# Kernel tuning notes

Measured on AMD Instinct MI355X. Metric: run time of the kernel, lower is better.

## Reference

```python
import jax, jax.numpy as jnp
import numpy as np

B, S, D, H, L = 32, 64, 8, 256, 2


def _lstm_layer(x, Wih, Whh, b):
    # x: (B, S, Hin) -> outputs (B, S, H), final h, c (B, H). PyTorch gate order i,f,g,o.
    Bsz = x.shape[0]
    Hd = Whh.shape[1]
    h0 = jnp.zeros((Bsz, Hd), x.dtype)
    c0 = jnp.zeros((Bsz, Hd), x.dtype)

    def step(carry, xt):
        h, c = carry
        g = xt @ Wih.T + h @ Whh.T + b
        i, f, gg, o = jnp.split(g, 4, axis=-1)
        c = jax.nn.sigmoid(f) * c + jax.nn.sigmoid(i) * jnp.tanh(gg)
        h = jax.nn.sigmoid(o) * jnp.tanh(c)
        return (h, c), h

    (hT, cT), ys = jax.lax.scan(step, (h0, c0), jnp.swapaxes(x, 0, 1))
    return jnp.swapaxes(ys, 0, 1), hT, cT


def _encode(x, layers):
    hs, cs = [], []
    out = x
    for (Wih, Whh, b) in layers:
        out, hT, cT = _lstm_layer(out, Wih, Whh, b)
        hs.append(hT)
        cs.append(cT)
    return out, jnp.stack(hs), jnp.stack(cs)  # out (B,S,H), h/c (L,B,H)


def _cell_step(x, h, c, layers):
    # single time-step through stacked LSTM. x (B,H); h,c (L,B,H)
    hs, cs = [], []
    inp = x
    for l, (Wih, Whh, b) in enumerate(layers):
        g = inp @ Wih.T + h[l] @ Whh.T + b
        i, f, gg, o = jnp.split(g, 4, axis=-1)
        cn = jax.nn.sigmoid(f) * c[l] + jax.nn.sigmoid(i) * jnp.tanh(gg)
        hn = jax.nn.sigmoid(o) * jnp.tanh(cn)
        hs.append(hn)
        cs.append(cn)
        inp = hn
    return inp, jnp.stack(hs), jnp.stack(cs)


def setup_inputs() -> dict:
    key = jax.random.key(0)
    ks = jax.random.split(key, 24)
    s = 0.05
    inputs = jax.random.uniform(ks[0], (B, S, D), dtype=jnp.float32)
    inputs = inputs.at[..., -1].set(0.0)  # is_visited flag starts at 0
    p = {}
    p['inputs'] = inputs
    p['W_emb'] = jax.random.normal(ks[1], (H, D), jnp.float32) * s
    p['b_emb'] = jax.random.normal(ks[2], (H,), jnp.float32) * s
    i = 3
    for pref, in0 in (('enc', H), ('dec', H)):
        for l in range(L):
            p[f'{pref}_Wih{l}'] = jax.random.normal(ks[i], (4 * H, in0 if l == 0 else H), jnp.float32) * s; i += 1
            p[f'{pref}_Whh{l}'] = jax.random.normal(ks[i], (4 * H, H), jnp.float32) * s; i += 1
            p[f'{pref}_b{l}'] = jax.random.normal(ks[i], (4 * H,), jnp.float32) * s; i += 1
    p['W1'] = jax.random.normal(ks[i], (H, H), jnp.float32) * s; i += 1
    p['W2'] = jax.random.normal(ks[i], (H, H), jnp.float32) * s; i += 1
    p['v'] = jax.random.normal(ks[i], (H,), jnp.float32) * s
    return p


def reference(inputs, W_emb, b_emb,
              enc_Wih0, enc_Whh0, enc_b0, enc_Wih1, enc_Whh1, enc_b1,
              dec_Wih0, dec_Whh0, dec_b0, dec_Wih1, dec_Whh1, dec_b1,
              W1, W2, v):
    # Eval-mode forward (dropout=identity, no teacher forcing): greedy pointer decode.
    enc_layers = [(enc_Wih0, enc_Whh0, enc_b0), (enc_Wih1, enc_Whh1, enc_b1)]
    dec_layers = [(dec_Wih0, dec_Whh0, dec_b0), (dec_Wih1, dec_Whh1, dec_b1)]
    Bsz, Sl, _ = inputs.shape
    batch_idx = jnp.arange(Bsz)

    def embed(ci):
        return jnp.tanh(ci @ W_emb.T + b_emb)

    # initial encode gives decoder init state and first decoder input
    enc0, h0, c0 = _encode(embed(inputs), enc_layers)
    dec_in0 = enc0[:, 0]  # (B, H)
    mask0 = jnp.zeros((Bsz, Sl), dtype=bool)

    def step(carry, _):
        cur, mask, h, c, dec_in = carry
        # re-encode mutated inputs every step (faithful to the original)
        enc_out, _, _ = _encode(embed(cur), enc_layers)
        dec_out, h, c = _cell_step(dec_in, h, c, dec_layers)
        # Bahdanau attention scores: v^T tanh(W1 e + W2 d)
        scores = jnp.tanh(enc_out @ W1.T + (dec_out @ W2.T)[:, None, :]) @ v  # (B, S)
        scores = jnp.where(mask, -jnp.inf, scores)
        pointer = jax.nn.softmax(scores, axis=1)
        index = jnp.argmax(pointer, axis=1)
        mask = mask.at[batch_idx, index].set(True)
        cur = cur.at[batch_idx, index, -1].set(1.0)  # mark visited
        dec_in = enc_out[batch_idx, index]  # gather next decoder input
        return (cur, mask, h, c, dec_in), (pointer, index)

    _, (pointers, indices) = jax.lax.scan(
        step, (inputs, mask0, h0, c0, dec_in0), None, length=Sl)
    pointers = jnp.swapaxes(pointers, 0, 1)  # (B, S, S)
    indices = jnp.swapaxes(indices, 0, 1)    # (B, S)
    return pointers, indices
```

## Files before the change

kernel.cpp:

```cpp
#include <hip/hip_runtime.h>
#include <math.h>

#define BB 32
#define SS 64
#define HH 256
#define G4 1024
#define NT 1024

#define W1T_OFF 2097152
#define W2T_OFF 2162688
#define PB_OFF  2228224
#define PBB     115712
#define OX1     0
#define OH1     65536
#define OP2     81920
#define OH2     98304
#define ODC1    114688
#define ODC2    114944
#define OEMB    115200
#define FLG_OFF (PB_OFF + 32*PBB)

__device__ __forceinline__ float sigmf(float x){ return 1.f/(1.f+expf(-x)); }
__device__ __forceinline__ float dot4(float4 a, float4 b){
  return fmaf(a.x,b.x,fmaf(a.y,b.y,fmaf(a.z,b.z,a.w*b.w)));
}
__device__ __forceinline__ void fst(unsigned* p, unsigned v){
  __hip_atomic_store(p, v, __ATOMIC_RELAXED, __HIP_MEMORY_SCOPE_AGENT);
}
__device__ __forceinline__ unsigned fld(unsigned* p){
  return __hip_atomic_load(p, __ATOMIC_RELAXED, __HIP_MEMORY_SCOPE_AGENT);
}
__device__ __forceinline__ void srel(float* p, float v){
  __hip_atomic_store(p, v, __ATOMIC_RELAXED, __HIP_MEMORY_SCOPE_AGENT);
}
__device__ __forceinline__ float lrel(const float* p){
  return __hip_atomic_load((float*)p, __ATOMIC_RELAXED, __HIP_MEMORY_SCOPE_AGENT);
}
__device__ __forceinline__ void drain_vm(){
  asm volatile("s_waitcnt vmcnt(0)" ::: "memory");
}
__device__ __forceinline__ int wait_ge(unsigned* p, unsigned want, unsigned* ab){
  int it = 0;
  for(;;){
    unsigned v = fld(p);
    if (v >= want) return (int)v;
    if ((++it & 2047) == 0){
      if (fld(ab) != 0u) return -1;
      if (it > (1<<23)){ fst(ab, 1u); return -1; }
    }
    __builtin_amdgcn_s_sleep(2);
  }
}

__global__ void zflags_k(float* ws){
  unsigned* f = (unsigned*)(ws + FLG_OFF);
  if (threadIdx.x < 512) f[threadIdx.x] = 0u;
}

__global__ void pack_transpose_k(const float* __restrict__ s0, const float* __restrict__ s1,
                                 const float* __restrict__ s2, const float* __restrict__ s3,
                                 const float* __restrict__ s4, const float* __restrict__ s5,
                                 const float* __restrict__ s6, const float* __restrict__ s7,
                                 float* __restrict__ ws) {
    __shared__ float tile[64][65];
    const float* srcs[8] = {s0, s1, s2, s3, s4, s5, s6, s7};
    const float* src = srcs[blockIdx.z];
    float* dst = ws + (size_t)blockIdx.z * (G4 * HH);
    int gblk = blockIdx.x * 64;
    int kblk = blockIdx.y * 64;
    for (int q = threadIdx.x; q < 64 * 64; q += 256) {
        int r = q >> 6, c = q & 63;
        tile[r][c] = src[(size_t)(gblk + r) * HH + (kblk + c)];
    }
    __syncthreads();
    for (int q = threadIdx.x; q < 64 * 64; q += 256) {
        int r = q & 3;
        int gl = (q >> 2) & 63;
        int k0l = q >> 8;
        int dsti = (((kblk >> 2) + k0l) * G4 + gblk + gl) * 4 + r;
        dst[dsti] = tile[gl][k0l * 4 + r];
    }
}

__global__ void transpose256_k(const float* __restrict__ W1, const float* __restrict__ W2,
                               float* __restrict__ ws) {
    __shared__ float tile[32][33];
    const float* src = blockIdx.z ? W2 : W1;
    float* dst = ws + (blockIdx.z ? W2T_OFF : W1T_OFF);
    int j0 = blockIdx.x * 32, k0 = blockIdx.y * 32;
    int tx = threadIdx.x & 31, ty = threadIdx.x >> 5;
    for (int i = ty; i < 32; i += 8) tile[i][tx] = src[(size_t)(j0 + i) * HH + k0 + tx];
    __syncthreads();
    for (int i = ty; i < 32; i += 8) dst[(size_t)(k0 + i) * HH + j0 + tx] = tile[tx][i];
}

__global__ void __launch_bounds__(NT) ptrnet_k(
    const float* __restrict__ inputs, const float* __restrict__ W_emb,
    const float* __restrict__ b_emb,
    const float* __restrict__ b_e0, const float* __restrict__ b_e1,
    const float* __restrict__ b_d0, const float* __restrict__ b_d1,
    const float* __restrict__ vv,
    float* __restrict__ ws, float* __restrict__ out) {
  const int g = blockIdx.x;
  const int role = g & 3;
  const int b = g >> 2;
  const int tid = threadIdx.x;

  const float4* ws4 = (const float4*)ws;
  const float4* We0ih = ws4 + 0*65536;
  const float4* We0hh = ws4 + 1*65536;
  const float4* We1ih = ws4 + 2*65536;
  const float4* We1hh = ws4 + 3*65536;
  const float4* Wd0ih = ws4 + 4*65536;
  const float4* Wd0hh = ws4 + 5*65536;
  const float4* Wd1ih = ws4 + 6*65536;
  const float4* Wd1hh = ws4 + 7*65536;
  const float* W1T = ws + W1T_OFF;
  const float* W2T = ws + W2T_OFF;

  float* pb   = ws + PB_OFF + (size_t)b * PBB;
  float* X1   = pb + OX1;
  float* h1cw = pb + OH1;
  float* p2cw = pb + OP2;
  float* h2cw = pb + OH2;
  float* dc1i = pb + ODC1;
  float* dc2i = pb + ODC2;
  float* embw = pb + OEMB;
  unsigned* flg = (unsigned*)(ws + FLG_OFF) + b*8;
  unsigned* abw = (unsigned*)(ws + FLG_OFF) + 256;

  __shared__ float big0[16384];
  __shared__ float big1[16384];
  __shared__ float gbuf[1024];
  __shared__ float v0[256], v1[256], v2[256], v3[256], v4[256], v5[256], v6[256];
  __shared__ float scr[64];
  __shared__ int msk[64];
  __shared__ int ibc[2];

  if (role == 0) {
    for (int i = tid; i < SS*HH; i += NT){
      int t = i >> 8, j = i & 255;
      const float* xr = inputs + ((size_t)b*SS + t)*8;
      float acc = b_emb[j];
#pragma unroll
      for (int d = 0; d < 8; ++d) acc = fmaf(xr[d], W_emb[j*8+d], acc);
      big0[i] = acc;
    }
    __syncthreads();
    for (int tile = 0; tile < 16; ++tile){
      { int tt = tid >> 8, j = tid & 255; gbuf[tid] = tanhf(big0[(tile*4+tt)*256 + j]); }
      __syncthreads();
      float a0=0.f,a1=0.f,a2=0.f,a3=0.f;
      for (int kq = 0; kq < 64; ++kq){
        float4 w = We0ih[(kq<<10) + tid];
        a0 += dot4(w, *(const float4*)&gbuf[   0 + kq*4]);
        a1 += dot4(w, *(const float4*)&gbuf[ 256 + kq*4]);
        a2 += dot4(w, *(const float4*)&gbuf[ 512 + kq*4]);
        a3 += dot4(w, *(const float4*)&gbuf[ 768 + kq*4]);
      }
      float bg = b_e0[tid];
      X1[(tile*4+0)*1024 + tid] = bg + a0;
      X1[(tile*4+1)*1024 + tid] = bg + a1;
      X1[(tile*4+2)*1024 + tid] = bg + a2;
      X1[(tile*4+3)*1024 + tid] = bg + a3;
      __syncthreads();
    }
    if (tid < 256) v0[tid] = 0.f;
    __syncthreads();
    int tau = 0;
    for (int p = 0; p < SS; ++p){
      int t0 = 0;
      if (p > 0){
        if (tid == 0){
          int iv = wait_ge(&flg[3], (unsigned)p << 8, abw);
          ibc[0] = (iv < 0) ? 0 : (iv & 255);
        }
        __syncthreads();
        t0 = ibc[0];
        if (tid < 256) v1[tid] = lrel(&embw[tid]);
        __syncthreads();
        { float acc = 0.f;
          for (int kq = 0; kq < 64; ++kq){
            float4 w = We0ih[(kq<<10) + tid];
            acc += dot4(w, *(const float4*)&v1[kq*4]);
          }
          X1[t0*1024 + tid] = b_e0[tid] + acc; }
        if (tid < 256) v0[tid] = (t0 > 0) ? lrel(&h1cw[(t0-1)*256 + tid]) : 0.f;
        __syncthreads();
      }
      for (int t = t0; t < SS; ++t){
        ++tau;
        { float acc = X1[t*1024 + tid];
          for (int kq = 0; kq < 64; ++kq){
            float4 w = We0hh[(kq<<10) + tid];
            acc += dot4(w, *(const float4*)&v0[kq*4]);
          }
          gbuf[tid] = acc; }
        __syncthreads();
        if (tid < 256){
          float Gi = gbuf[tid], Gf = gbuf[tid+256], Gg = gbuf[tid+512], Go = gbuf[tid+768];
          float cp = (t == 0) ? 0.f : big0[(t-1)*256 + tid];
          float cc = sigmf(Gf)*cp + sigmf(Gi)*tanhf(Gg);
          float hh = sigmf(Go)*tanhf(cc);
          big0[t*256 + tid] = cc; v0[tid] = hh;
          srel(&h1cw[t*256 + tid], hh);
          if (p == 0 && t == SS-1) srel(&dc1i[tid], cc);
        }
        drain_vm();
        __syncthreads();
        if (tid == 0) fst(&flg[0], (unsigned)tau);
      }
    }
  }
  else if (role == 1) {
    int tau = 0;
    for (int p = 0; p < SS; ++p){
      int t0 = 0;
      if (p > 0){
        if (tid == 0){
          int iv = wait_ge(&flg[3], (unsigned)p << 8, abw);
          ibc[0] = (iv < 0) ? 0 : (iv & 255);
        }
        __syncthreads();
        t0 = ibc[0];
      }
      for (int t = t0; t < SS; ++t){
        ++tau;
        if (tid == 0){
          wait_ge(&flg[0], (unsigned)tau, abw);
          if (tau > 16) wait_ge(&flg[2], (unsigned)(tau-16), abw);
        }
        __syncthreads();
        if (tid < 256) v0[tid] = lrel(&h1cw[t*256 + tid]);
        __syncthreads();
        float acc = b_e1[tid];
        for (int kq = 0; kq < 64; ++kq){
          float4 w = We1ih[(kq<<10) + tid];
          acc += dot4(w, *(const float4*)&v0[kq*4]);
        }
        srel(&p2cw[(tau & 15)*1024 + tid], acc);
        drain_vm();
        __syncthreads();
        if (tid == 0) fst(&flg[1], (unsigned)tau);
      }
    }
  }
  else if (role == 2) {
    int tau = 0;
    for (int p = 0; p < SS; ++p){
      int t0 = 0;
      if (p > 0){
        if (tid == 0){
          int iv = wait_ge(&flg[3], (unsigned)p << 8, abw);
          ibc[0] = (iv < 0) ? 0 : (iv & 255);
        }
        __syncthreads();
        t0 = ibc[0];
      }
      if (tid < 256) v0[tid] = (t0 > 0) ? lrel(&h2cw[(t0-1)*256 + tid]) : 0.f;
      __syncthreads();
      for (int t = t0; t < SS; ++t){
        ++tau;
        if (tid == 0) wait_ge(&flg[1], (unsigned)tau, abw);
        __syncthreads();
        float acc = lrel(&p2cw[(tau & 15)*1024 + tid]);
        for (int kq = 0; kq < 64; ++kq){
          float4 w = We1hh[(kq<<10) + tid];
          acc += dot4(w, *(const float4*)&v0[kq*4]);
        }
        gbuf[tid] = acc;
        __syncthreads();
        if (tid < 256){
          float Gi = gbuf[tid], Gf = gbuf[tid+256], Gg = gbuf[tid+512], Go = gbuf[tid+768];
          float cp = (t == 0) ? 0.f : big0[(t-1)*256 + tid];
          float cc = sigmf(Gf)*cp + sigmf(Gi)*tanhf(Gg);
          float hh = sigmf(Go)*tanhf(cc);
          big0[t*256 + tid] = cc; v0[tid] = hh;
          srel(&h2cw[t*256 + tid], hh);
          if (p == 0 && t == SS-1) srel(&dc2i[tid], cc);
        }
        drain_vm();
        __syncthreads();
        if (tid == 0) fst(&flg[2], (unsigned)tau);
      }
    }
  }
  else {
    for (int i = tid; i < SS*HH; i += NT){
      int t = i >> 8, j = i & 255;
      const float* xr = inputs + ((size_t)b*SS + t)*8;
      float acc = b_emb[j];
#pragma unroll
      for (int d = 0; d < 8; ++d) acc = fmaf(xr[d], W_emb[j*8+d], acc);
      big0[i] = acc;
    }
    if (tid < 64) msk[tid] = 0;
    __syncthreads();

    auto dec_cell = [&](){
      { float acc = b_d0[tid];
        for (int kq = 0; kq < 64; ++kq){
          acc += dot4(Wd0ih[(kq<<10) + tid], *(const float4*)&v2[kq*4]);
          acc += dot4(Wd0hh[(kq<<10) + tid], *(const float4*)&v3[kq*4]);
        }
        gbuf[tid] = acc; }
      __syncthreads();
      if (tid < 256){
        float Gi = gbuf[tid], Gf = gbuf[tid+256], Gg = gbuf[tid+512], Go = gbuf[tid+768];
        float cc = sigmf(Gf)*v4[tid] + sigmf(Gi)*tanhf(Gg);
        float hh = sigmf(Go)*tanhf(cc);
        v4[tid] = cc; v3[tid] = hh;
      }
      __syncthreads();
      { float acc = b_d1[tid];
        for (int kq = 0; kq < 64; ++kq){
          acc += dot4(Wd1ih[(kq<<10) + tid], *(const float4*)&v3[kq*4]);
          acc += dot4(Wd1hh[(kq<<10) + tid], *(const float4*)&v5[kq*4]);
        }
        gbuf[tid] = acc; }
      __syncthreads();
      if (tid < 256){
        float Gi = gbuf[tid], Gf = gbuf[tid+256], Gg = gbuf[tid+512], Go = gbuf[tid+768];
        float cc = sigmf(Gf)*v6[tid] + sigmf(Gi)*tanhf(Gg);
        float hh = sigmf(Go)*tanhf(cc);
        v6[tid] = cc; v5[tid] = hh;
      }
      __syncthreads();
      { int j = tid & 255, c = tid >> 8;
        float a = 0.f;
        for (int k = c*64; k < c*64 + 64; ++k) a = fmaf(v5[k], W2T[k*256 + j], a);
        gbuf[tid] = a; }
      __syncthreads();
      if (tid < 256) v1[tid] = gbuf[tid] + gbuf[tid+256] + gbuf[tid+512] + gbuf[tid+768];
      __syncthreads();
    };

    int tau = 0, lastidx = 0;
    for (int p = 0; p < SS; ++p){
      int t0 = (p == 0) ? 0 : lastidx;
      if (p > 0) dec_cell();
      for (int t = t0; t < SS; ++t){
        ++tau;
        if (tid == 0) wait_ge(&flg[2], (unsigned)tau, abw);
        __syncthreads();
        if (tid < 256) v0[tid] = lrel(&h2cw[t*256 + tid]);
        __syncthreads();
        { int j = tid & 255, c = tid >> 8;
          float a = 0.f;
          for (int k = c*64; k < c*64 + 64; ++k) a = fmaf(v0[k], W1T[k*256 + j], a);
          gbuf[tid] = a; }
        __syncthreads();
        if (tid < 256) big1[t*256 + tid] = gbuf[tid] + gbuf[tid+256] + gbuf[tid+512] + gbuf[tid+768];
        __syncthreads();
      }
      if (p == 0){
        if (tid < 256){
          v3[tid] = lrel(&h1cw[63*256 + tid]);
          v4[tid] = lrel(&dc1i[tid]);
          v5[tid] = lrel(&h2cw[63*256 + tid]);
          v6[tid] = lrel(&dc2i[tid]);
          v2[tid] = lrel(&h2cw[0*256 + tid]);
        }
        __syncthreads();
        dec_cell();
      }
      { int t = tid >> 4, r = tid & 15;
        float a = 0.f;
        for (int j = r; j < HH; j += 16) a += vv[j] * tanhf(big1[t*256 + j] + v1[j]);
        a += __shfl_xor(a, 8, 16);
        a += __shfl_xor(a, 4, 16);
        a += __shfl_xor(a, 2, 16);
        a += __shfl_xor(a, 1, 16);
        if (r == 0) scr[t] = msk[t] ? -3.0e38f : a; }
      __syncthreads();
      if (tid < SS){
        float sv = scr[tid];
        float m = sv; int mi = tid;
#pragma unroll
        for (int o = 32; o >= 1; o >>= 1){
          float ov = __shfl_xor(m, o, 64);
          int oi = __shfl_xor(mi, o, 64);
          if (ov > m || (ov == m && oi < mi)){ m = ov; mi = oi; }
        }
        float e = expf(sv - m);
        float ssum = e;
#pragma unroll
        for (int o = 32; o >= 1; o >>= 1) ssum += __shfl_xor(ssum, o, 64);
        out[((size_t)b*SS + p)*SS + tid] = e / ssum;
        if (tid == 0){
          msk[mi] = 1;
          out[(size_t)BB*SS*SS + (size_t)b*SS + p] = (float)mi;
          ibc[1] = mi;
        }
      }
      __syncthreads();
      int idx = ibc[1];
      lastidx = idx;
      if (p < SS-1){
        if (tid < 256){
          v2[tid] = lrel(&h2cw[idx*256 + tid]);
          float e = tanhf(big0[idx*256 + tid] + W_emb[tid*8 + 7]);
          srel(&embw[tid], e);
        }
        drain_vm();
        __syncthreads();
        if (tid == 0) fst(&flg[3], ((unsigned)(p+1) << 8) | (unsigned)idx);
      }
    }
  }
}

extern "C" void kernel_launch(void* const* d_in, const int* in_sizes, int n_in,
                              void* d_out, int out_size, void* d_ws, size_t ws_size,
                              hipStream_t stream) {
  const float* inputs = (const float*)d_in[0];
  const float* W_emb  = (const float*)d_in[1];
  const float* b_emb  = (const float*)d_in[2];
  const float* e_Wih0 = (const float*)d_in[3];
  const float* e_Whh0 = (const float*)d_in[4];
  const float* e_b0   = (const float*)d_in[5];
  const float* e_Wih1 = (const float*)d_in[6];
  const float* e_Whh1 = (const float*)d_in[7];
  const float* e_b1   = (const float*)d_in[8];
  const float* d_Wih0 = (const float*)d_in[9];
  const float* d_Whh0 = (const float*)d_in[10];
  const float* d_b0   = (const float*)d_in[11];
  const float* d_Wih1 = (const float*)d_in[12];
  const float* d_Whh1 = (const float*)d_in[13];
  const float* d_b1   = (const float*)d_in[14];
  const float* W1     = (const float*)d_in[15];
  const float* W2     = (const float*)d_in[16];
  const float* v      = (const float*)d_in[17];
  float* ws  = (float*)d_ws;
  float* out = (float*)d_out;

  zflags_k<<<dim3(1), dim3(512), 0, stream>>>(ws);
  pack_transpose_k<<<dim3(16, 4, 8), dim3(256), 0, stream>>>(
      e_Wih0, e_Whh0, e_Wih1, e_Whh1, d_Wih0, d_Whh0, d_Wih1, d_Whh1, ws);
  transpose256_k<<<dim3(8, 8, 2), dim3(256), 0, stream>>>(W1, W2, ws);
  ptrnet_k<<<dim3(BB*4), dim3(NT), 0, stream>>>(
      inputs, W_emb, b_emb, e_b0, e_b1, d_b0, d_b1, v, ws, out);
}
```

Baseline: 23.09 ms.

## Split encoder LSTM layers across two half-hidden workgroups with peer flag sync

Each encoder role (layer-0 recurrence, layer-1 input projection, layer-1 recurrence) now runs on two 512-thread workgroups, each owning half of the hidden units. The halves exchange h through global memory with per-step peer flags, and each half computes its own-half dot products before waiting on the peer. The grid grows from 4 to 8 blocks per batch item (one idle), the weight pack layout is changed to match, and the spin-wait sleep is shortened. The goal is to shorten the serial per-timestep recurrence latency, at the cost of an extra cross-workgroup handshake on every step and a 512-thread decoder.

```diff
diff --git a/kernel.cpp b/kernel.cpp
--- a/kernel.cpp
+++ b/kernel.cpp
@@ -4,8 +4,7 @@
 #define BB 32
 #define SS 64
 #define HH 256
-#define G4 1024
-#define NT 1024
+#define NT 512
 
 #define W1T_OFF 2097152
 #define W2T_OFF 2162688
@@ -19,6 +18,14 @@
 #define ODC2    114944
 #define OEMB    115200
 #define FLG_OFF (PB_OFF + 32*PBB)
+#define FA0 0
+#define FA1 32
+#define FB0 64
+#define FB1 96
+#define FC0 128
+#define FC1 160
+#define FD  192
+#define NFLGW (32*256 + 32)
 
 __device__ __forceinline__ float sigmf(float x){ return 1.f/(1.f+expf(-x)); }
 __device__ __forceinline__ float dot4(float4 a, float4 b){
@@ -48,50 +55,49 @@
       if (fld(ab) != 0u) return -1;
       if (it > (1<<23)){ fst(ab, 1u); return -1; }
     }
-    __builtin_amdgcn_s_sleep(2);
+    __builtin_amdgcn_s_sleep(1);
   }
 }
 
 __global__ void zflags_k(float* ws){
   unsigned* f = (unsigned*)(ws + FLG_OFF);
-  if (threadIdx.x < 512) f[threadIdx.x] = 0u;
-}
-
-__global__ void pack_transpose_k(const float* __restrict__ s0, const float* __restrict__ s1,
-                                 const float* __restrict__ s2, const float* __restrict__ s3,
-                                 const float* __restrict__ s4, const float* __restrict__ s5,
-                                 const float* __restrict__ s6, const float* __restrict__ s7,
-                                 float* __restrict__ ws) {
-    __shared__ float tile[64][65];
-    const float* srcs[8] = {s0, s1, s2, s3, s4, s5, s6, s7};
-    const float* src = srcs[blockIdx.z];
-    float* dst = ws + (size_t)blockIdx.z * (G4 * HH);
-    int gblk = blockIdx.x * 64;
-    int kblk = blockIdx.y * 64;
-    for (int q = threadIdx.x; q < 64 * 64; q += 256) {
-        int r = q >> 6, c = q & 63;
-        tile[r][c] = src[(size_t)(gblk + r) * HH + (kblk + c)];
-    }
-    __syncthreads();
-    for (int q = threadIdx.x; q < 64 * 64; q += 256) {
-        int r = q & 3;
-        int gl = (q >> 2) & 63;
-        int k0l = q >> 8;
-        int dsti = (((kblk >> 2) + k0l) * G4 + gblk + gl) * 4 + r;
-        dst[dsti] = tile[gl][k0l * 4 + r];
-    }
+  int i = blockIdx.x*1024 + threadIdx.x;
+  if (i < NFLGW) f[i] = 0u;
+}
+
+__global__ void pack_k(const float* __restrict__ e0ih, const float* __restrict__ e0hh,
+                       const float* __restrict__ e1ih, const float* __restrict__ e1hh,
+                       const float* __restrict__ d0ih, const float* __restrict__ d0hh,
+                       const float* __restrict__ d1ih, const float* __restrict__ d1hh,
+                       float* __restrict__ ws){
+  const float* encm[4] = {e0ih,e0hh,e1ih,e1hh};
+  const float* decm[4] = {d0ih,d0hh,d1ih,d1hh};
+  float4* dst = (float4*)ws;
+  int gid = blockIdx.x*256 + threadIdx.x;
+  if (gid < 262144){
+    int mx = gid >> 15, rem = gid & 32767;
+    int kq = rem >> 9, r = rem & 511;
+    int m = mx >> 1, x = mx & 1;
+    int grow = ((r>>7)<<8) + (x<<7) + (r&127);
+    dst[gid] = *(const float4*)&encm[m][(size_t)grow*256 + kq*4];
+  } else {
+    int g2 = gid - 262144;
+    int m = g2 >> 16, rem = g2 & 65535;
+    int kq = rem >> 10, row = rem & 1023;
+    dst[gid] = *(const float4*)&decm[m][(size_t)row*256 + kq*4];
+  }
 }
 
 __global__ void transpose256_k(const float* __restrict__ W1, const float* __restrict__ W2,
                                float* __restrict__ ws) {
-    __shared__ float tile[32][33];
-    const float* src = blockIdx.z ? W2 : W1;
-    float* dst = ws + (blockIdx.z ? W2T_OFF : W1T_OFF);
-    int j0 = blockIdx.x * 32, k0 = blockIdx.y * 32;
-    int tx = threadIdx.x & 31, ty = threadIdx.x >> 5;
-    for (int i = ty; i < 32; i += 8) tile[i][tx] = src[(size_t)(j0 + i) * HH + k0 + tx];
-    __syncthreads();
-    for (int i = ty; i < 32; i += 8) dst[(size_t)(k0 + i) * HH + j0 + tx] = tile[tx][i];
+  __shared__ float tile[32][33];
+  const float* src = blockIdx.z ? W2 : W1;
+  float* dst = ws + (blockIdx.z ? W2T_OFF : W1T_OFF);
+  int j0 = blockIdx.x * 32, k0 = blockIdx.y * 32;
+  int tx = threadIdx.x & 31, ty = threadIdx.x >> 5;
+  for (int i = ty; i < 32; i += 8) tile[i][tx] = src[(size_t)(j0 + i) * HH + k0 + tx];
+  __syncthreads();
+  for (int i = ty; i < 32; i += 8) dst[(size_t)(k0 + i) * HH + j0 + tx] = tile[tx][i];
 }
 
 __global__ void __launch_bounds__(NT) ptrnet_k(
@@ -102,42 +108,46 @@
     const float* __restrict__ vv,
     float* __restrict__ ws, float* __restrict__ out) {
   const int g = blockIdx.x;
-  const int role = g & 3;
-  const int b = g >> 2;
+  const int role = g & 7;
+  const int b = g >> 3;
   const int tid = threadIdx.x;
+  if (role == 7) return;
 
   const float4* ws4 = (const float4*)ws;
-  const float4* We0ih = ws4 + 0*65536;
-  const float4* We0hh = ws4 + 1*65536;
-  const float4* We1ih = ws4 + 2*65536;
-  const float4* We1hh = ws4 + 3*65536;
-  const float4* Wd0ih = ws4 + 4*65536;
-  const float4* Wd0hh = ws4 + 5*65536;
-  const float4* Wd1ih = ws4 + 6*65536;
-  const float4* Wd1hh = ws4 + 7*65536;
   const float* W1T = ws + W1T_OFF;
   const float* W2T = ws + W2T_OFF;
 
   float* pb   = ws + PB_OFF + (size_t)b * PBB;
-  float* X1   = pb + OX1;
   float* h1cw = pb + OH1;
-  float* p2cw = pb + OP2;
   float* h2cw = pb + OH2;
   float* dc1i = pb + ODC1;
   float* dc2i = pb + ODC2;
   float* embw = pb + OEMB;
-  unsigned* flg = (unsigned*)(ws + FLG_OFF) + b*8;
-  unsigned* abw = (unsigned*)(ws + FLG_OFF) + 256;
+  unsigned* W = (unsigned*)(ws + FLG_OFF);
+  unsigned* flg = W + b*256;
+  unsigned* abw = W + 32*256;
 
   __shared__ float big0[16384];
   __shared__ float big1[16384];
-  __shared__ float gbuf[1024];
-  __shared__ float v0[256], v1[256], v2[256], v3[256], v4[256], v5[256], v6[256];
+  __shared__ float gb2[2048];
+  __shared__ float gbuf[512];
+  __shared__ __align__(16) float vA[128], vB[128];
+  __shared__ __align__(16) float v0[256], v1[256], v2[256], v3[256], v4[256], v5[256], v6[256];
   __shared__ float scr[64];
   __shared__ int msk[64];
   __shared__ int ibc[2];
 
-  if (role == 0) {
+  if (role < 2) {
+    const int x = role, px = 1 - x;
+    const float4* Wih = ws4 + (0*2 + x)*32768;
+    const float4* Whh = ws4 + (1*2 + x)*32768;
+    float* X1x = pb + OX1 + x*32768;
+    const int r = tid;
+    const int grow = ((r>>7)<<8) + (x<<7) + (r&127);
+    const float be0r = b_e0[grow];
+    unsigned* myF = &flg[x ? FA1 : FA0];
+    unsigned* peF = &flg[x ? FA0 : FA1];
+
     for (int i = tid; i < SS*HH; i += NT){
       int t = i >> 8, j = i & 255;
       const float* xr = inputs + ((size_t)b*SS + t)*8;
@@ -147,78 +157,135 @@
       big0[i] = acc;
     }
     __syncthreads();
-    for (int tile = 0; tile < 16; ++tile){
-      { int tt = tid >> 8, j = tid & 255; gbuf[tid] = tanhf(big0[(tile*4+tt)*256 + j]); }
-      __syncthreads();
-      float a0=0.f,a1=0.f,a2=0.f,a3=0.f;
+    for (int tile = 0; tile < 8; ++tile){
+      for (int i = tid; i < 2048; i += NT){
+        int tt = i >> 8, j = i & 255;
+        gb2[i] = tanhf(big0[(tile*8+tt)*256 + j]);
+      }
+      __syncthreads();
+      float a[8] = {0,0,0,0,0,0,0,0};
       for (int kq = 0; kq < 64; ++kq){
-        float4 w = We0ih[(kq<<10) + tid];
-        a0 += dot4(w, *(const float4*)&gbuf[   0 + kq*4]);
-        a1 += dot4(w, *(const float4*)&gbuf[ 256 + kq*4]);
-        a2 += dot4(w, *(const float4*)&gbuf[ 512 + kq*4]);
-        a3 += dot4(w, *(const float4*)&gbuf[ 768 + kq*4]);
-      }
-      float bg = b_e0[tid];
-      X1[(tile*4+0)*1024 + tid] = bg + a0;
-      X1[(tile*4+1)*1024 + tid] = bg + a1;
-      X1[(tile*4+2)*1024 + tid] = bg + a2;
-      X1[(tile*4+3)*1024 + tid] = bg + a3;
-      __syncthreads();
-    }
-    if (tid < 256) v0[tid] = 0.f;
-    __syncthreads();
+        float4 w = Wih[(kq<<9) + r];
+#pragma unroll
+        for (int tt = 0; tt < 8; ++tt) a[tt] += dot4(w, *(const float4*)&gb2[tt*256 + kq*4]);
+      }
+#pragma unroll
+      for (int tt = 0; tt < 8; ++tt) X1x[(tile*8+tt)*512 + r] = be0r + a[tt];
+      __syncthreads();
+    }
+    int tau = 0;
+    for (int p = 0; p < SS; ++p){
+      int t0 = 0;
+      float x1t0 = 0.f; bool fuse = false;
+      if (p > 0){
+        if (tid == 0){
+          int iv = wait_ge(&flg[FD], (unsigned)p << 8, abw);
+          ibc[0] = (iv < 0) ? 0 : (iv & 255);
+        }
+        __syncthreads();
+        t0 = ibc[0];
+        if (tid < 256) v1[tid] = lrel(&embw[tid]);
+        __syncthreads();
+        float accR = be0r;
+        for (int kq = 0; kq < 64; ++kq)
+          accR += dot4(Wih[(kq<<9) + r], *(const float4*)&v1[kq*4]);
+        X1x[t0*512 + r] = accR;
+        x1t0 = accR; fuse = true;
+      }
+      for (int t = t0; t < SS; ++t){
+        ++tau;
+        if (t == t0){
+          if (tid < 128){
+            float a0 = 0.f, b0 = 0.f;
+            if (t0 > 0){
+              a0 = lrel(&h1cw[(t0-1)*256 + x*128 + tid]);
+              b0 = lrel(&h1cw[(t0-1)*256 + px*128 + tid]);
+            }
+            vA[tid] = a0; vB[tid] = b0;
+          }
+          __syncthreads();
+        }
+        float acc = (fuse && t == t0) ? x1t0 : X1x[t*512 + r];
+        for (int kq = x*32; kq < x*32+32; ++kq)
+          acc += dot4(Whh[(kq<<9) + r], *(const float4*)&vA[(kq - x*32)*4]);
+        if (t > t0){
+          if (tid == 0) wait_ge(peF, (unsigned)(tau-1), abw);
+          __syncthreads();
+          if (tid < 128) vB[tid] = lrel(&h1cw[(t-1)*256 + px*128 + tid]);
+          __syncthreads();
+        }
+        for (int kq = px*32; kq < px*32+32; ++kq)
+          acc += dot4(Whh[(kq<<9) + r], *(const float4*)&vB[(kq - px*32)*4]);
+        gbuf[r] = acc;
+        __syncthreads();
+        if (tid < 128){
+          float Gi = gbuf[tid], Gf = gbuf[128+tid], Gg = gbuf[256+tid], Go = gbuf[384+tid];
+          float cp = (t == 0) ? 0.f : big0[(t-1)*128 + tid];
+          float cc = sigmf(Gf)*cp + sigmf(Gi)*tanhf(Gg);
+          float hh = sigmf(Go)*tanhf(cc);
+          big0[t*128 + tid] = cc; vA[tid] = hh;
+          srel(&h1cw[t*256 + x*128 + tid], hh);
+          if (p == 0 && t == SS-1) srel(&dc1i[x*128 + tid], cc);
+        }
+        drain_vm();
+        __syncthreads();
+        if (tid == 0) fst(myF, (unsigned)tau);
+      }
+    }
+  }
+  else if (role < 4) {
+    const int x = role - 2;
+    const float4* Wih1 = ws4 + (2*2 + x)*32768;
+    float* p2x = pb + OP2 + x*8192;
+    const int r = tid;
+    const float be1r = b_e1[((r>>7)<<8) + (x<<7) + (r&127)];
+    unsigned* fC = &flg[x ? FC1 : FC0];
+    unsigned* fB = &flg[x ? FB1 : FB0];
     int tau = 0;
     for (int p = 0; p < SS; ++p){
       int t0 = 0;
       if (p > 0){
         if (tid == 0){
-          int iv = wait_ge(&flg[3], (unsigned)p << 8, abw);
+          int iv = wait_ge(&flg[FD], (unsigned)p << 8, abw);
           ibc[0] = (iv < 0) ? 0 : (iv & 255);
         }
         __syncthreads();
         t0 = ibc[0];
-        if (tid < 256) v1[tid] = lrel(&embw[tid]);
-        __syncthreads();
-        { float acc = 0.f;
-          for (int kq = 0; kq < 64; ++kq){
-            float4 w = We0ih[(kq<<10) + tid];
-            acc += dot4(w, *(const float4*)&v1[kq*4]);
-          }
-          X1[t0*1024 + tid] = b_e0[tid] + acc; }
-        if (tid < 256) v0[tid] = (t0 > 0) ? lrel(&h1cw[(t0-1)*256 + tid]) : 0.f;
-        __syncthreads();
       }
       for (int t = t0; t < SS; ++t){
         ++tau;
-        { float acc = X1[t*1024 + tid];
-          for (int kq = 0; kq < 64; ++kq){
-            float4 w = We0hh[(kq<<10) + tid];
-            acc += dot4(w, *(const float4*)&v0[kq*4]);
-          }
-          gbuf[tid] = acc; }
-        __syncthreads();
-        if (tid < 256){
-          float Gi = gbuf[tid], Gf = gbuf[tid+256], Gg = gbuf[tid+512], Go = gbuf[tid+768];
-          float cp = (t == 0) ? 0.f : big0[(t-1)*256 + tid];
-          float cc = sigmf(Gf)*cp + sigmf(Gi)*tanhf(Gg);
-          float hh = sigmf(Go)*tanhf(cc);
-          big0[t*256 + tid] = cc; v0[tid] = hh;
-          srel(&h1cw[t*256 + tid], hh);
-          if (p == 0 && t == SS-1) srel(&dc1i[tid], cc);
-        }
+        if (tid == 0){
+          wait_ge(&flg[FA0], (unsigned)tau, abw);
+          wait_ge(&flg[FA1], (unsigned)tau, abw);
+          if (tau > 16) wait_ge(fC, (unsigned)(tau-16), abw);
+        }
+        __syncthreads();
+        if (tid < 256) v0[tid] = lrel(&h1cw[t*256 + tid]);
+        __syncthreads();
+        float acc = be1r;
+        for (int kq = 0; kq < 64; ++kq)
+          acc += dot4(Wih1[(kq<<9) + r], *(const float4*)&v0[kq*4]);
+        srel(&p2x[(tau & 15)*512 + r], acc);
         drain_vm();
         __syncthreads();
-        if (tid == 0) fst(&flg[0], (unsigned)tau);
+        if (tid == 0) fst(fB, (unsigned)tau);
       }
     }
   }
-  else if (role == 1) {
+  else if (role < 6) {
+    const int x = role - 4, px = 1 - x;
+    const float4* Whh1 = ws4 + (3*2 + x)*32768;
+    float* p2x = pb + OP2 + x*8192;
+    const int r = tid;
+    unsigned* myF = &flg[x ? FC1 : FC0];
+    unsigned* peF = &flg[x ? FC0 : FC1];
+    unsigned* fB = &flg[x ? FB1 : FB0];
     int tau = 0;
     for (int p = 0; p < SS; ++p){
       int t0 = 0;
       if (p > 0){
         if (tid == 0){
-          int iv = wait_ge(&flg[3], (unsigned)p << 8, abw);
+          int iv = wait_ge(&flg[FD], (unsigned)p << 8, abw);
           ibc[0] = (iv < 0) ? 0 : (iv & 255);
         }
         __syncthreads();
@@ -226,66 +293,54 @@
       }
       for (int t = t0; t < SS; ++t){
         ++tau;
-        if (tid == 0){
-          wait_ge(&flg[0], (unsigned)tau, abw);
-          if (tau > 16) wait_ge(&flg[2], (unsigned)(tau-16), abw);
-        }
-        __syncthreads();
-        if (tid < 256) v0[tid] = lrel(&h1cw[t*256 + tid]);
-        __syncthreads();
-        float acc = b_e1[tid];
-        for (int kq = 0; kq < 64; ++kq){
-          float4 w = We1ih[(kq<<10) + tid];
-          acc += dot4(w, *(const float4*)&v0[kq*4]);
-        }
-        srel(&p2cw[(tau & 15)*1024 + tid], acc);
-        drain_vm();
-        __syncthreads();
-        if (tid == 0) fst(&flg[1], (unsigned)tau);
-      }
-    }
-  }
-  else if (role == 2) {
-    int tau = 0;
-    for (int p = 0; p < SS; ++p){
-      int t0 = 0;
-      if (p > 0){
-        if (tid == 0){
-          int iv = wait_ge(&flg[3], (unsigned)p << 8, abw);
-          ibc[0] = (iv < 0) ? 0 : (iv & 255);
-        }
-        __syncthreads();
-        t0 = ibc[0];
-      }
-      if (tid < 256) v0[tid] = (t0 > 0) ? lrel(&h2cw[(t0-1)*256 + tid]) : 0.f;
-      __syncthreads();
-      for (int t = t0; t < SS; ++t){
-        ++tau;
-        if (tid == 0) wait_ge(&flg[1], (unsigned)tau, abw);
-        __syncthreads();
-        float acc = lrel(&p2cw[(tau & 15)*1024 + tid]);
-        for (int kq = 0; kq < 64; ++kq){
-          float4 w = We1hh[(kq<<10) + tid];
-          acc += dot4(w, *(const float4*)&v0[kq*4]);
-        }
-        gbuf[tid] = acc;
-        __syncthreads();
-        if (tid < 256){
-          float Gi = gbuf[tid], Gf = gbuf[tid+256], Gg = gbuf[tid+512], Go = gbuf[tid+768];
-          float cp = (t == 0) ? 0.f : big0[(t-1)*256 + tid];
+        if (t == t0){
+          if (tid < 128){
+            float a0 = 0.f, b0 = 0.f;
+            if (t0 > 0){
+              a0 = lrel(&h2cw[(t0-1)*256 + x*128 + tid]);
+              b0 = lrel(&h2cw[(t0-1)*256 + px*128 + tid]);
+            }
+            vA[tid] = a0; vB[tid] = b0;
+          }
+          __syncthreads();
+        }
+        float acc = 0.f;
+        for (int kq = x*32; kq < x*32+32; ++kq)
+          acc += dot4(Whh1[(kq<<9) + r], *(const float4*)&vA[(kq - x*32)*4]);
+        if (tid == 0){
+          wait_ge(fB, (unsigned)tau, abw);
+          if (t > t0) wait_ge(peF, (unsigned)(tau-1), abw);
+        }
+        __syncthreads();
+        if (t > t0){
+          if (tid < 128) vB[tid] = lrel(&h2cw[(t-1)*256 + px*128 + tid]);
+        }
+        float p2v = lrel(&p2x[(tau & 15)*512 + r]);
+        __syncthreads();
+        for (int kq = px*32; kq < px*32+32; ++kq)
+          acc += dot4(Whh1[(kq<<9) + r], *(const float4*)&vB[(kq - px*32)*4]);
+        gbuf[r] = acc + p2v;
+        __syncthreads();
+        if (tid < 128){
+          float Gi = gbuf[tid], Gf = gbuf[128+tid], Gg = gbuf[256+tid], Go = gbuf[384+tid];
+          float cp = (t == 0) ? 0.f : big0[(t-1)*128 + tid];
           float cc = sigmf(Gf)*cp + sigmf(Gi)*tanhf(Gg);
           float hh = sigmf(Go)*tanhf(cc);
-          big0[t*256 + tid] = cc; v0[tid] = hh;
-          srel(&h2cw[t*256 + tid], hh);
-          if (p == 0 && t == SS-1) srel(&dc2i[tid], cc);
+          big0[t*128 + tid] = cc; vA[tid] = hh;
+          srel(&h2cw[t*256 + x*128 + tid], hh);
+          if (p == 0 && t == SS-1) srel(&dc2i[x*128 + tid], cc);
         }
         drain_vm();
         __syncthreads();
-        if (tid == 0) fst(&flg[2], (unsigned)tau);
+        if (tid == 0) fst(myF, (unsigned)tau);
       }
     }
   }
   else {
+    const float4* WD0ih = ws4 + 262144 + 0*65536;
+    const float4* WD0hh = ws4 + 262144 + 1*65536;
+    const float4* WD1ih = ws4 + 262144 + 2*65536;
+    const float4* WD1hh = ws4 + 262144 + 3*65536;
     for (int i = tid; i < SS*HH; i += NT){
       int t = i >> 8, j = i & 255;
       const float* xr = inputs + ((size_t)b*SS + t)*8;
@@ -298,29 +353,37 @@
     __syncthreads();
 
     auto dec_cell = [&](){
-      { float acc = b_d0[tid];
+#pragma unroll
+      for (int h = 0; h < 2; ++h){
+        int row = h*512 + tid;
+        float acc = b_d0[row];
         for (int kq = 0; kq < 64; ++kq){
-          acc += dot4(Wd0ih[(kq<<10) + tid], *(const float4*)&v2[kq*4]);
-          acc += dot4(Wd0hh[(kq<<10) + tid], *(const float4*)&v3[kq*4]);
-        }
-        gbuf[tid] = acc; }
+          acc += dot4(WD0ih[(kq<<10) + row], *(const float4*)&v2[kq*4]);
+          acc += dot4(WD0hh[(kq<<10) + row], *(const float4*)&v3[kq*4]);
+        }
+        gb2[row] = acc;
+      }
       __syncthreads();
       if (tid < 256){
-        float Gi = gbuf[tid], Gf = gbuf[tid+256], Gg = gbuf[tid+512], Go = gbuf[tid+768];
+        float Gi = gb2[tid], Gf = gb2[256+tid], Gg = gb2[512+tid], Go = gb2[768+tid];
         float cc = sigmf(Gf)*v4[tid] + sigmf(Gi)*tanhf(Gg);
         float hh = sigmf(Go)*tanhf(cc);
         v4[tid] = cc; v3[tid] = hh;
       }
       __syncthreads();
-      { float acc = b_d1[tid];
+#pragma unroll
+      for (int h = 0; h < 2; ++h){
+        int row = h*512 + tid;
+        float acc = b_d1[row];
         for (int kq = 0; kq < 64; ++kq){
-          acc += dot4(Wd1ih[(kq<<10) + tid], *(const float4*)&v3[kq*4]);
-          acc += dot4(Wd1hh[(kq<<10) + tid], *(const float4*)&v5[kq*4]);
-        }
-        gbuf[tid] = acc; }
+          acc += dot4(WD1ih[(kq<<10) + row], *(const float4*)&v3[kq*4]);
+          acc += dot4(WD1hh[(kq<<10) + row], *(const float4*)&v5[kq*4]);
+        }
+        gb2[row] = acc;
+      }
       __syncthreads();
       if (tid < 256){
-        float Gi = gbuf[tid], Gf = gbuf[tid+256], Gg = gbuf[tid+512], Go = gbuf[tid+768];
+        float Gi = gb2[tid], Gf = gb2[256+tid], Gg = gb2[512+tid], Go = gb2[768+tid];
         float cc = sigmf(Gf)*v6[tid] + sigmf(Gi)*tanhf(Gg);
         float hh = sigmf(Go)*tanhf(cc);
         v6[tid] = cc; v5[tid] = hh;
@@ -328,10 +391,10 @@
       __syncthreads();
       { int j = tid & 255, c = tid >> 8;
         float a = 0.f;
-        for (int k = c*64; k < c*64 + 64; ++k) a = fmaf(v5[k], W2T[k*256 + j], a);
+        for (int k = c*128; k < c*128 + 128; ++k) a = fmaf(v5[k], W2T[k*256 + j], a);
         gbuf[tid] = a; }
       __syncthreads();
-      if (tid < 256) v1[tid] = gbuf[tid] + gbuf[tid+256] + gbuf[tid+512] + gbuf[tid+768];
+      if (tid < 256) v1[tid] = gbuf[tid] + gbuf[256+tid];
       __syncthreads();
     };
 
@@ -341,16 +404,19 @@
       if (p > 0) dec_cell();
       for (int t = t0; t < SS; ++t){
         ++tau;
-        if (tid == 0) wait_ge(&flg[2], (unsigned)tau, abw);
+        if (tid == 0){
+          wait_ge(&flg[FC0], (unsigned)tau, abw);
+          wait_ge(&flg[FC1], (unsigned)tau, abw);
+        }
         __syncthreads();
         if (tid < 256) v0[tid] = lrel(&h2cw[t*256 + tid]);
         __syncthreads();
         { int j = tid & 255, c = tid >> 8;
           float a = 0.f;
-          for (int k = c*64; k < c*64 + 64; ++k) a = fmaf(v0[k], W1T[k*256 + j], a);
+          for (int k = c*128; k < c*128 + 128; ++k) a = fmaf(v0[k], W1T[k*256 + j], a);
           gbuf[tid] = a; }
         __syncthreads();
-        if (tid < 256) big1[t*256 + tid] = gbuf[tid] + gbuf[tid+256] + gbuf[tid+512] + gbuf[tid+768];
+        if (tid < 256) big1[t*256 + tid] = gbuf[tid] + gbuf[256+tid];
         __syncthreads();
       }
       if (p == 0){
@@ -364,14 +430,13 @@
         __syncthreads();
         dec_cell();
       }
-      { int t = tid >> 4, r = tid & 15;
+      { int t = tid >> 3, r8 = tid & 7;
         float a = 0.f;
-        for (int j = r; j < HH; j += 16) a += vv[j] * tanhf(big1[t*256 + j] + v1[j]);
-        a += __shfl_xor(a, 8, 16);
-        a += __shfl_xor(a, 4, 16);
-        a += __shfl_xor(a, 2, 16);
-        a += __shfl_xor(a, 1, 16);
-        if (r == 0) scr[t] = msk[t] ? -3.0e38f : a; }
+        for (int j = r8; j < HH; j += 8) a += vv[j] * tanhf(big1[t*256 + j] + v1[j]);
+        a += __shfl_xor(a, 4, 8);
+        a += __shfl_xor(a, 2, 8);
+        a += __shfl_xor(a, 1, 8);
+        if (r8 == 0) scr[t] = msk[t] ? -3.0e38f : a; }
       __syncthreads();
       if (tid < SS){
         float sv = scr[tid];
@@ -404,7 +469,7 @@
         }
         drain_vm();
         __syncthreads();
-        if (tid == 0) fst(&flg[3], ((unsigned)(p+1) << 8) | (unsigned)idx);
+        if (tid == 0) fst(&flg[FD], ((unsigned)(p+1) << 8) | (unsigned)idx);
       }
     }
   }
@@ -434,10 +499,10 @@
   float* ws  = (float*)d_ws;
   float* out = (float*)d_out;
 
-  zflags_k<<<dim3(1), dim3(512), 0, stream>>>(ws);
-  pack_transpose_k<<<dim3(16, 4, 8), dim3(256), 0, stream>>>(
+  zflags_k<<<dim3(9), dim3(1024), 0, stream>>>(ws);
+  pack_k<<<dim3(2048), dim3(256), 0, stream>>>(
       e_Wih0, e_Whh0, e_Wih1, e_Whh1, d_Wih0, d_Whh0, d_Wih1, d_Whh1, ws);
   transpose256_k<<<dim3(8, 8, 2), dim3(256), 0, stream>>>(W1, W2, ws);
-  ptrnet_k<<<dim3(BB*4), dim3(NT), 0, stream>>>(
+  ptrnet_k<<<dim3(BB*8), dim3(NT), 0, stream>>>(
       inputs, W_emb, b_emb, e_b0, e_b1, d_b0, d_b1, v, ws, out);
 }
```

New measurement: 33.10 ms. +43.4%, slower.

## Precompute visited-flag layer-0 input projections and pad flags to separate cache lines

Applied to the files above, without the earlier changes.

During the prologue, the layer-0 encoder block now also computes the input projection of every timestep as if its visited flag were set, and stores it in a new workspace buffer X1B. After each pointer step it reads the precomputed row instead of waiting on the decoder to publish a tanh embedding and then doing a 256x1024 matvec on the critical path. The embedding write is dropped from the attention role, and the per-batch flags are spread to separate 128-byte slots to avoid false sharing. This doubles the prologue matvec work and adds a 8MB buffer, with a fallback path when the workspace is too small.

```diff
diff --git a/kernel.cpp b/kernel.cpp
--- a/kernel.cpp
+++ b/kernel.cpp
@@ -17,8 +17,13 @@
 #define OH2     98304
 #define ODC1    114688
 #define ODC2    114944
-#define OEMB    115200
 #define FLG_OFF (PB_OFF + 32*PBB)
+#define NFLGW   (32*256 + 32)
+#define X1B_OFF (FLG_OFF + NFLGW)
+#define FA 0
+#define FB 32
+#define FC 64
+#define FD 96
 
 __device__ __forceinline__ float sigmf(float x){ return 1.f/(1.f+expf(-x)); }
 __device__ __forceinline__ float dot4(float4 a, float4 b){
@@ -54,7 +59,8 @@
 
 __global__ void zflags_k(float* ws){
   unsigned* f = (unsigned*)(ws + FLG_OFF);
-  if (threadIdx.x < 512) f[threadIdx.x] = 0u;
+  int i = blockIdx.x*1024 + threadIdx.x;
+  if (i < NFLGW) f[i] = 0u;
 }
 
 __global__ void pack_transpose_k(const float* __restrict__ s0, const float* __restrict__ s1,
@@ -100,7 +106,7 @@
     const float* __restrict__ b_e0, const float* __restrict__ b_e1,
     const float* __restrict__ b_d0, const float* __restrict__ b_d1,
     const float* __restrict__ vv,
-    float* __restrict__ ws, float* __restrict__ out) {
+    float* __restrict__ ws, float* __restrict__ out, int useX1B) {
   const int g = blockIdx.x;
   const int role = g & 3;
   const int b = g >> 2;
@@ -125,9 +131,10 @@
   float* h2cw = pb + OH2;
   float* dc1i = pb + ODC1;
   float* dc2i = pb + ODC2;
-  float* embw = pb + OEMB;
-  unsigned* flg = (unsigned*)(ws + FLG_OFF) + b*8;
-  unsigned* abw = (unsigned*)(ws + FLG_OFF) + 256;
+  float* X1B  = ws + X1B_OFF + (size_t)b * 65536;
+  unsigned* Wf  = (unsigned*)(ws + FLG_OFF);
+  unsigned* flg = Wf + b*256;
+  unsigned* abw = Wf + 32*256;
 
   __shared__ float big0[16384];
   __shared__ float big1[16384];
@@ -148,21 +155,35 @@
     }
     __syncthreads();
     for (int tile = 0; tile < 16; ++tile){
-      { int tt = tid >> 8, j = tid & 255; gbuf[tid] = tanhf(big0[(tile*4+tt)*256 + j]); }
+      { int tt = tid >> 8, j = tid & 255;
+        float pe = big0[(tile*4+tt)*256 + j];
+        gbuf[tid] = tanhf(pe);
+        big1[tid] = tanhf(pe + W_emb[j*8 + 7]); }
       __syncthreads();
       float a0=0.f,a1=0.f,a2=0.f,a3=0.f;
+      float c0=0.f,c1=0.f,c2=0.f,c3=0.f;
       for (int kq = 0; kq < 64; ++kq){
         float4 w = We0ih[(kq<<10) + tid];
         a0 += dot4(w, *(const float4*)&gbuf[   0 + kq*4]);
         a1 += dot4(w, *(const float4*)&gbuf[ 256 + kq*4]);
         a2 += dot4(w, *(const float4*)&gbuf[ 512 + kq*4]);
         a3 += dot4(w, *(const float4*)&gbuf[ 768 + kq*4]);
+        c0 += dot4(w, *(const float4*)&big1[   0 + kq*4]);
+        c1 += dot4(w, *(const float4*)&big1[ 256 + kq*4]);
+        c2 += dot4(w, *(const float4*)&big1[ 512 + kq*4]);
+        c3 += dot4(w, *(const float4*)&big1[ 768 + kq*4]);
       }
       float bg = b_e0[tid];
       X1[(tile*4+0)*1024 + tid] = bg + a0;
       X1[(tile*4+1)*1024 + tid] = bg + a1;
       X1[(tile*4+2)*1024 + tid] = bg + a2;
       X1[(tile*4+3)*1024 + tid] = bg + a3;
+      if (useX1B){
+        X1B[(tile*4+0)*1024 + tid] = bg + c0;
+        X1B[(tile*4+1)*1024 + tid] = bg + c1;
+        X1B[(tile*4+2)*1024 + tid] = bg + c2;
+        X1B[(tile*4+3)*1024 + tid] = bg + c3;
+      }
       __syncthreads();
     }
     if (tid < 256) v0[tid] = 0.f;
@@ -170,32 +191,41 @@
     int tau = 0;
     for (int p = 0; p < SS; ++p){
       int t0 = 0;
+      float xr0 = 0.f;
       if (p > 0){
         if (tid == 0){
-          int iv = wait_ge(&flg[3], (unsigned)p << 8, abw);
+          int iv = wait_ge(&flg[FD], (unsigned)p << 8, abw);
           ibc[0] = (iv < 0) ? 0 : (iv & 255);
         }
         __syncthreads();
         t0 = ibc[0];
-        if (tid < 256) v1[tid] = lrel(&embw[tid]);
-        __syncthreads();
-        { float acc = 0.f;
-          for (int kq = 0; kq < 64; ++kq){
-            float4 w = We0ih[(kq<<10) + tid];
-            acc += dot4(w, *(const float4*)&v1[kq*4]);
+        if (useX1B){
+          xr0 = X1B[t0*1024 + tid];
+        } else {
+          if (tid < 256){
+            const float* xr = inputs + ((size_t)b*SS + t0)*8;
+            float pe = b_emb[tid];
+#pragma unroll
+            for (int d = 0; d < 8; ++d) pe = fmaf(xr[d], W_emb[tid*8+d], pe);
+            v1[tid] = tanhf(pe + W_emb[tid*8 + 7]);
           }
-          X1[t0*1024 + tid] = b_e0[tid] + acc; }
+          __syncthreads();
+          float accR = 0.f;
+          for (int kq = 0; kq < 64; ++kq)
+            accR += dot4(We0ih[(kq<<10) + tid], *(const float4*)&v1[kq*4]);
+          xr0 = b_e0[tid] + accR;
+        }
+        X1[t0*1024 + tid] = xr0;
         if (tid < 256) v0[tid] = (t0 > 0) ? lrel(&h1cw[(t0-1)*256 + tid]) : 0.f;
         __syncthreads();
       }
       for (int t = t0; t < SS; ++t){
         ++tau;
-        { float acc = X1[t*1024 + tid];
-          for (int kq = 0; kq < 64; ++kq){
-            float4 w = We0hh[(kq<<10) + tid];
-            acc += dot4(w, *(const float4*)&v0[kq*4]);
-          }
-          gbuf[tid] = acc; }
+        float xv = (p > 0 && t == t0) ? xr0 : X1[t*1024 + tid];
+        float acc = 0.f;
+        for (int kq = 0; kq < 64; ++kq)
+          acc += dot4(We0hh[(kq<<10) + tid], *(const float4*)&v0[kq*4]);
+        gbuf[tid] = acc + xv;
         __syncthreads();
         if (tid < 256){
           float Gi = gbuf[tid], Gf = gbuf[tid+256], Gg = gbuf[tid+512], Go = gbuf[tid+768];
@@ -208,7 +238,7 @@
         }
         drain_vm();
         __syncthreads();
-        if (tid == 0) fst(&flg[0], (unsigned)tau);
+        if (tid == 0) fst(&flg[FA], (unsigned)tau);
       }
     }
   }
@@ -218,7 +248,7 @@
       int t0 = 0;
       if (p > 0){
         if (tid == 0){
-          int iv = wait_ge(&flg[3], (unsigned)p << 8, abw);
+          int iv = wait_ge(&flg[FD], (unsigned)p << 8, abw);
           ibc[0] = (iv < 0) ? 0 : (iv & 255);
         }
         __syncthreads();
@@ -227,21 +257,19 @@
       for (int t = t0; t < SS; ++t){
         ++tau;
         if (tid == 0){
-          wait_ge(&flg[0], (unsigned)tau, abw);
-          if (tau > 16) wait_ge(&flg[2], (unsigned)(tau-16), abw);
+          wait_ge(&flg[FA], (unsigned)tau, abw);
+          if (tau > 16) wait_ge(&flg[FC], (unsigned)(tau-16), abw);
         }
         __syncthreads();
         if (tid < 256) v0[tid] = lrel(&h1cw[t*256 + tid]);
         __syncthreads();
         float acc = b_e1[tid];
-        for (int kq = 0; kq < 64; ++kq){
-          float4 w = We1ih[(kq<<10) + tid];
-          acc += dot4(w, *(const float4*)&v0[kq*4]);
-        }
+        for (int kq = 0; kq < 64; ++kq)
+          acc += dot4(We1ih[(kq<<10) + tid], *(const float4*)&v0[kq*4]);
         srel(&p2cw[(tau & 15)*1024 + tid], acc);
         drain_vm();
         __syncthreads();
-        if (tid == 0) fst(&flg[1], (unsigned)tau);
+        if (tid == 0) fst(&flg[FB], (unsigned)tau);
       }
     }
   }
@@ -251,7 +279,7 @@
       int t0 = 0;
       if (p > 0){
         if (tid == 0){
-          int iv = wait_ge(&flg[3], (unsigned)p << 8, abw);
+          int iv = wait_ge(&flg[FD], (unsigned)p << 8, abw);
           ibc[0] = (iv < 0) ? 0 : (iv & 255);
         }
         __syncthreads();
@@ -261,14 +289,13 @@
       __syncthreads();
       for (int t = t0; t < SS; ++t){
         ++tau;
-        if (tid == 0) wait_ge(&flg[1], (unsigned)tau, abw);
-        __syncthreads();
-        float acc = lrel(&p2cw[(tau & 15)*1024 + tid]);
-        for (int kq = 0; kq < 64; ++kq){
-          float4 w = We1hh[(kq<<10) + tid];
-          acc += dot4(w, *(const float4*)&v0[kq*4]);
-        }
-        gbuf[tid] = acc;
+        if (tid == 0) wait_ge(&flg[FB], (unsigned)tau, abw);
+        __syncthreads();
+        float p2v = lrel(&p2cw[(tau & 15)*1024 + tid]);
+        float acc = 0.f;
+        for (int kq = 0; kq < 64; ++kq)
+          acc += dot4(We1hh[(kq<<10) + tid], *(const float4*)&v0[kq*4]);
+        gbuf[tid] = acc + p2v;
         __syncthreads();
         if (tid < 256){
           float Gi = gbuf[tid], Gf = gbuf[tid+256], Gg = gbuf[tid+512], Go = gbuf[tid+768];
@@ -281,7 +308,7 @@
         }
         drain_vm();
         __syncthreads();
-        if (tid == 0) fst(&flg[2], (unsigned)tau);
+        if (tid == 0) fst(&flg[FC], (unsigned)tau);
       }
     }
   }
@@ -341,7 +368,7 @@
       if (p > 0) dec_cell();
       for (int t = t0; t < SS; ++t){
         ++tau;
-        if (tid == 0) wait_ge(&flg[2], (unsigned)tau, abw);
+        if (tid == 0) wait_ge(&flg[FC], (unsigned)tau, abw);
         __syncthreads();
         if (tid < 256) v0[tid] = lrel(&h2cw[t*256 + tid]);
         __syncthreads();
@@ -397,14 +424,10 @@
       int idx = ibc[1];
       lastidx = idx;
       if (p < SS-1){
-        if (tid < 256){
-          v2[tid] = lrel(&h2cw[idx*256 + tid]);
-          float e = tanhf(big0[idx*256 + tid] + W_emb[tid*8 + 7]);
-          srel(&embw[tid], e);
-        }
+        if (tid < 256) v2[tid] = lrel(&h2cw[idx*256 + tid]);
         drain_vm();
         __syncthreads();
-        if (tid == 0) fst(&flg[3], ((unsigned)(p+1) << 8) | (unsigned)idx);
+        if (tid == 0) fst(&flg[FD], ((unsigned)(p+1) << 8) | (unsigned)idx);
       }
     }
   }
@@ -434,10 +457,13 @@
   float* ws  = (float*)d_ws;
   float* out = (float*)d_out;
 
-  zflags_k<<<dim3(1), dim3(512), 0, stream>>>(ws);
+  size_t need = ((size_t)X1B_OFF + 32u*65536u) * 4u;
+  int useX1B = (ws_size >= need) ? 1 : 0;
+
+  zflags_k<<<dim3(9), dim3(1024), 0, stream>>>(ws);
   pack_transpose_k<<<dim3(16, 4, 8), dim3(256), 0, stream>>>(
       e_Wih0, e_Whh0, e_Wih1, e_Whh1, d_Wih0, d_Whh0, d_Wih1, d_Whh1, ws);
   transpose256_k<<<dim3(8, 8, 2), dim3(256), 0, stream>>>(W1, W2, ws);
   ptrnet_k<<<dim3(BB*4), dim3(NT), 0, stream>>>(
-      inputs, W_emb, b_emb, e_b0, e_b1, d_b0, d_b1, v, ws, out);
-}
+      inputs, W_emb, b_emb, e_b0, e_b1, d_b0, d_b1, v, ws, out, useX1B);
+}
```

After: 22.12 ms (median of 2 runs). -4.2%, faster.
